# Kernel optimization log

Measured on AMD Instinct MI355X. Metric: run time of the kernel, lower is better.

The kernel has to match this reference:

```python
import jax, jax.numpy as jnp
import numpy as np
import math

D_MODEL = 1024
NUM_HEADS = 16
D_K = D_MODEL // NUM_HEADS
SEQ = 4096
THETA = 10000.0


def _rope_tables(d_k, max_seq_len, theta):
    freqs = 1.0 / theta ** (jnp.arange(0, d_k, 2, dtype=jnp.float32) / d_k)  # (d_k/2,)
    pos = jnp.arange(max_seq_len, dtype=jnp.float32)
    ang = pos[:, None] * freqs[None, :]  # (S, d_k/2)
    return jnp.cos(ang), jnp.sin(ang)


def setup_inputs() -> dict:
    key = jax.random.key(0)
    ks = jax.random.split(key, 5)
    std = math.sqrt(2.0 / (D_MODEL + D_MODEL))
    def trunc_w(k):
        return jax.random.truncated_normal(k, -3.0, 3.0, (D_MODEL, D_MODEL), jnp.float32) * std
    x = jax.random.normal(ks[0], (1, SEQ, D_MODEL), jnp.float32)
    Wq, Wk, Wv, Wo = trunc_w(ks[1]), trunc_w(ks[2]), trunc_w(ks[3]), trunc_w(ks[4])
    cos, sin = _rope_tables(D_K, SEQ, THETA)
    positions = jnp.arange(SEQ, dtype=jnp.int32)
    return {"x": x, "Wq": Wq, "Wk": Wk, "Wv": Wv, "Wo": Wo,
            "cos": cos, "sin": sin, "positions": positions}


def _apply_rope(t, cos, sin, positions):
    # t: (b, h, s, d_k); cos/sin: (max_s, d_k/2)
    c = cos[positions][None, None]  # (1,1,s,d_k/2)
    s = sin[positions][None, None]
    x1, x2 = t[..., ::2], t[..., 1::2]
    rotated = jnp.stack([x1 * c - x2 * s, x1 * s + x2 * c], axis=-1)  # (b,h,s,d_k/2,2)
    return rotated.reshape(t.shape)


def reference(x, Wq, Wk, Wv, Wo, cos, sin, positions):
    b, s, d = x.shape
    h, dk = NUM_HEADS, D_K
    def proj(W):
        y = jnp.einsum('bsi,oi->bso', x, W)
        return y.reshape(b, s, h, dk).transpose(0, 2, 1, 3)  # (b,h,s,dk)
    Q, K, V = proj(Wq), proj(Wk), proj(Wv)
    Q = _apply_rope(Q, cos, sin, positions)
    K = _apply_rope(K, cos, sin, positions)
    scores = jnp.einsum('bhqd,bhkd->bhqk', Q, K) / math.sqrt(dk)
    causal = jnp.tril(jnp.ones((s, s), dtype=bool))
    scores = jnp.where(causal[None, None], scores, -jnp.inf)
    weights = jax.nn.softmax(scores, axis=-1)
    y = jnp.einsum('bhqk,bhkd->bhqd', weights, V)
    y = y.transpose(0, 2, 1, 3).reshape(b, s, d)
    return jnp.einsum('bsi,oi->bso', y, Wo)
```

## Files before the change

### kernel.cpp

```cpp
#include <hip/hip_runtime.h>
#include <math.h>

#define SEQ 4096
#define DM  1024
#define NH  16
#define DK  64

typedef __attribute__((ext_vector_type(4))) float f32x4;
typedef __attribute__((ext_vector_type(8))) short bf16x8;
typedef __attribute__((ext_vector_type(8))) unsigned short u16x8;

union FragU { u16x8 u; bf16x8 b; ushort4 q[2]; unsigned w[4]; };

__device__ __forceinline__ unsigned cvtpk(float a, float b) {
    unsigned r; asm("v_cvt_pk_bf16_f32 %0, %1, %2" : "=v"(r) : "v"(a), "v"(b)); return r;
}
__device__ __forceinline__ float fexp2(float x) {
    float r; asm("v_exp_f32 %0, %1" : "=v"(r) : "v"(x)); return r;
}
__device__ __forceinline__ void split4(float4 v, ushort4& hv, ushort4& lv) {
    union { ushort4 q; unsigned w[2]; } H, L;
    H.w[0] = cvtpk(v.x, v.y); H.w[1] = cvtpk(v.z, v.w);
    const float rx = v.x - __uint_as_float(H.w[0] << 16);
    const float ry = v.y - __uint_as_float(H.w[0] & 0xffff0000u);
    const float rz = v.z - __uint_as_float(H.w[1] << 16);
    const float rw = v.w - __uint_as_float(H.w[1] & 0xffff0000u);
    L.w[0] = cvtpk(rx, ry); L.w[1] = cvtpk(rz, rw);
    hv = H.q; lv = L.q;
}
__device__ __forceinline__ void split1(float f, unsigned short& h, unsigned short& l) {
    const unsigned hw = cvtpk(f, f) & 0xffffu;
    h = (unsigned short)hw;
    const float r = f - __uint_as_float(hw << 16);
    l = (unsigned short)(__float_as_uint(r) >> 16);
}

template<int MODE>
__global__ __launch_bounds__(256, 2)
void gemm_mfma(const float* __restrict__ Af,
               const unsigned short* __restrict__ Ahi, const unsigned short* __restrict__ Alo,
               const float* __restrict__ W0, const float* __restrict__ W1,
               const float* __restrict__ W2,
               unsigned short* __restrict__ OQh, unsigned short* __restrict__ OQl,
               unsigned short* __restrict__ OKh, unsigned short* __restrict__ OKl,
               unsigned short* __restrict__ OVh, unsigned short* __restrict__ OVl,
               float* __restrict__ Ofp,
               const float* __restrict__ cosT, const float* __restrict__ sinT,
               const int* __restrict__ positions)
{
    constexpr int NT = (MODE == 4) ? 24 : 8;
    __shared__ unsigned short As[128][76];
    __shared__ unsigned short Bs[128][76];

    const int t   = threadIdx.x;
    const int bid = blockIdx.x;
    const int qpx = (32 * NT) >> 3;
    const int swz = (bid & 7) * qpx + (bid >> 3);
    const int by  = swz / NT;
    const int bxf = swz % NT;
    const int wt  = (MODE == 4) ? (bxf >> 3) : 0;
    const int bx  = (MODE == 4) ? (bxf & 7) : bxf;
    const int m0  = by * 128;
    const float* W = (MODE == 4) ? (wt == 0 ? W0 : (wt == 1 ? W1 : W2)) : W0;

    const int lane = t & 63, w = t >> 6;
    const int wr = w >> 1, wc = w & 1;
    const int l15 = lane & 15, lg = lane >> 4;

    const int ar = t >> 1, ah = t & 1;
    const float* Ap = (MODE == 4) ? &Af[(size_t)(m0 + ar) * DM + ah * 16] : nullptr;
    const unsigned short* Aph = (MODE == 0) ? &Ahi[(size_t)(m0 + ar) * DM + ah * 16] : nullptr;
    const unsigned short* Apl = (MODE == 0) ? &Alo[(size_t)(m0 + ar) * DM + ah * 16] : nullptr;
    const float* Wp = &W[(size_t)(bx * 128 + ar) * DM + ah * 16];

    f32x4 acc[4][4];
#pragma unroll
    for (int mi = 0; mi < 4; ++mi)
#pragma unroll
        for (int ni = 0; ni < 4; ++ni) acc[mi][ni] = (f32x4){0.f, 0.f, 0.f, 0.f};

    float4 pa[4], pb[4];
    u16x8 pah[2], pal[2];
    if constexpr (MODE == 4) {
#pragma unroll
        for (int g = 0; g < 4; ++g) pa[g] = *reinterpret_cast<const float4*>(Ap + g * 4);
    } else {
        pah[0] = *reinterpret_cast<const u16x8*>(Aph);
        pah[1] = *reinterpret_cast<const u16x8*>(Aph + 8);
        pal[0] = *reinterpret_cast<const u16x8*>(Apl);
        pal[1] = *reinterpret_cast<const u16x8*>(Apl + 8);
    }
#pragma unroll
    for (int g = 0; g < 4; ++g) pb[g] = *reinterpret_cast<const float4*>(Wp + g * 4);

    for (int kt = 0; kt < 32; ++kt) {
        if constexpr (MODE == 4) {
#pragma unroll
            for (int g = 0; g < 4; ++g) {
                ushort4 hv, lv;
                split4(pa[g], hv, lv);
                *reinterpret_cast<ushort4*>(&As[ar][8 * g + 4 * ah])      = hv;
                *reinterpret_cast<ushort4*>(&As[ar][32 + 8 * g + 4 * ah]) = lv;
            }
        } else {
            FragU h0, h1, l0, l1;
            h0.u = pah[0]; h1.u = pah[1]; l0.u = pal[0]; l1.u = pal[1];
            *reinterpret_cast<ushort4*>(&As[ar][0  + 4 * ah]) = h0.q[0];
            *reinterpret_cast<ushort4*>(&As[ar][8  + 4 * ah]) = h0.q[1];
            *reinterpret_cast<ushort4*>(&As[ar][16 + 4 * ah]) = h1.q[0];
            *reinterpret_cast<ushort4*>(&As[ar][24 + 4 * ah]) = h1.q[1];
            *reinterpret_cast<ushort4*>(&As[ar][32 + 4 * ah]) = l0.q[0];
            *reinterpret_cast<ushort4*>(&As[ar][40 + 4 * ah]) = l0.q[1];
            *reinterpret_cast<ushort4*>(&As[ar][48 + 4 * ah]) = l1.q[0];
            *reinterpret_cast<ushort4*>(&As[ar][56 + 4 * ah]) = l1.q[1];
        }
#pragma unroll
        for (int g = 0; g < 4; ++g) {
            ushort4 hv, lv;
            split4(pb[g], hv, lv);
            *reinterpret_cast<ushort4*>(&Bs[ar][8 * g + 4 * ah])      = hv;
            *reinterpret_cast<ushort4*>(&Bs[ar][32 + 8 * g + 4 * ah]) = lv;
        }
        __syncthreads();

        if (kt < 31) {
            const int ko = (kt + 1) * 32;
            if constexpr (MODE == 4) {
#pragma unroll
                for (int g = 0; g < 4; ++g)
                    pa[g] = *reinterpret_cast<const float4*>(Ap + ko + g * 4);
            } else {
                pah[0] = *reinterpret_cast<const u16x8*>(Aph + ko);
                pah[1] = *reinterpret_cast<const u16x8*>(Aph + ko + 8);
                pal[0] = *reinterpret_cast<const u16x8*>(Apl + ko);
                pal[1] = *reinterpret_cast<const u16x8*>(Apl + ko + 8);
            }
#pragma unroll
            for (int g = 0; g < 4; ++g)
                pb[g] = *reinterpret_cast<const float4*>(Wp + ko + g * 4);
        }

        FragU b_h[4], b_l[4];
#pragma unroll
        for (int ni = 0; ni < 4; ++ni) {
            const int row = wc * 64 + ni * 16 + l15;
            b_h[ni].u = *reinterpret_cast<const u16x8*>(&Bs[row][8 * lg]);
            b_l[ni].u = *reinterpret_cast<const u16x8*>(&Bs[row][32 + 8 * lg]);
        }
#pragma unroll
        for (int mi = 0; mi < 4; ++mi) {
            FragU a_h, a_l;
            const int row = wr * 64 + mi * 16 + l15;
            a_h.u = *reinterpret_cast<const u16x8*>(&As[row][8 * lg]);
            a_l.u = *reinterpret_cast<const u16x8*>(&As[row][32 + 8 * lg]);
#pragma unroll
            for (int ni = 0; ni < 4; ++ni) {
                f32x4 c = acc[mi][ni];
                c = __builtin_amdgcn_mfma_f32_16x16x32_bf16(a_h.b, b_h[ni].b, c, 0, 0, 0);
                c = __builtin_amdgcn_mfma_f32_16x16x32_bf16(a_h.b, b_l[ni].b, c, 0, 0, 0);
                c = __builtin_amdgcn_mfma_f32_16x16x32_bf16(a_l.b, b_h[ni].b, c, 0, 0, 0);
                acc[mi][ni] = c;
            }
        }
        __syncthreads();
    }

    if constexpr (MODE == 0) {
#pragma unroll
        for (int mi = 0; mi < 4; ++mi)
#pragma unroll
            for (int ni = 0; ni < 4; ++ni)
#pragma unroll
                for (int r = 0; r < 4; ++r) {
                    const int m = m0 + wr * 64 + mi * 16 + lg * 4 + r;
                    const int n = bx * 128 + wc * 64 + ni * 16 + l15;
                    Ofp[(size_t)m * DM + n] = acc[mi][ni][r];
                }
    } else if (wt == 2) {
#pragma unroll
        for (int mi = 0; mi < 4; ++mi)
#pragma unroll
            for (int ni = 0; ni < 4; ++ni) {
                ushort4 hv, lv;
                unsigned short* hp = (unsigned short*)&hv;
                unsigned short* lp = (unsigned short*)&lv;
#pragma unroll
                for (int r = 0; r < 4; ++r) split1(acc[mi][ni][r], hp[r], lp[r]);
                const int vrow = bx * 128 + wc * 64 + ni * 16 + l15;
                const size_t off = (size_t)vrow * SEQ + m0 + wr * 64 + mi * 16 + lg * 4;
                *reinterpret_cast<ushort4*>(&OVh[off]) = hv;
                *reinterpret_cast<ushort4*>(&OVl[off]) = lv;
            }
    } else {
        unsigned short* Oh = (wt == 0) ? OQh : OKh;
        unsigned short* Ol = (wt == 0) ? OQl : OKl;
        const int head = bx * 2 + wc;
        const float qsc = 0.1803368801f;
#pragma unroll
        for (int mi = 0; mi < 4; ++mi)
#pragma unroll
            for (int r = 0; r < 4; ++r) {
                const int m   = m0 + wr * 64 + mi * 16 + lg * 4 + r;
                const int pos = positions[m];
#pragma unroll
                for (int ni = 0; ni < 4; ++ni) {
                    float val = acc[mi][ni][r];
                    const int d = ni * 16 + l15;
                    const float other = __shfl_xor(val, 1);
                    const float cc = cosT[pos * 32 + ni * 8 + (l15 >> 1)];
                    const float ss = sinT[pos * 32 + ni * 8 + (l15 >> 1)];
                    val = (d & 1) ? fmaf(other, ss, val * cc)
                                  : fmaf(other, -ss, val * cc);
                    if (wt == 0) val *= qsc;
                    unsigned short hh, ll;
                    split1(val, hh, ll);
                    const size_t off = ((size_t)head * SEQ + m) * DK + d;
                    Oh[off] = hh; Ol[off] = ll;
                }
            }
    }
}

__global__ __launch_bounds__(256, 1)
void attn_mfma(const unsigned short* __restrict__ Qhi, const unsigned short* __restrict__ Qlo,
               const unsigned short* __restrict__ Khi, const unsigned short* __restrict__ Klo,
               const unsigned short* __restrict__ Vhi, const unsigned short* __restrict__ Vlo,
               unsigned short* __restrict__ Yh, unsigned short* __restrict__ Yl)
{
    __shared__ unsigned short KsH[64][72], KsL[64][72];
    __shared__ unsigned short VsH[64][72], VsL[64][72];

    const int t = threadIdx.x, lane = t & 63, w = t >> 6;
    const int bid = blockIdx.x;
    const int xcd = bid & 7, idx = bid >> 3;
    const int h = 2 * xcd + (idx >> 4);
    const int pairI = idx & 15;
    const int l15 = lane & 15, lg = lane >> 4, dg = lg * 4;
    const int srow = t >> 2, q16 = t & 3;
    const int sc0 = (q16 >> 1) * 32 + 4 * (q16 & 1);

    u16x8 pf[8];

#pragma unroll 1
    for (int pass = 0; pass < 2; ++pass) {
        const int qt = pass ? (31 - pairI) : pairI;
        const int K0 = 2 * qt;
        const int ktmax = K0 + 1;

        bf16x8 qh[2][2], ql[2][2];
#pragma unroll
        for (int u = 0; u < 2; ++u) {
            const size_t qrow = ((size_t)h * SEQ + (size_t)qt * 128 + u * 64 + w * 16 + l15) * DK;
#pragma unroll
            for (int c = 0; c < 2; ++c) {
                FragU uh, ul;
                uh.q[0] = *reinterpret_cast<const ushort4*>(&Qhi[qrow + c * 32 + dg]);
                uh.q[1] = *reinterpret_cast<const ushort4*>(&Qhi[qrow + c * 32 + 16 + dg]);
                ul.q[0] = *reinterpret_cast<const ushort4*>(&Qlo[qrow + c * 32 + dg]);
                ul.q[1] = *reinterpret_cast<const ushort4*>(&Qlo[qrow + c * 32 + 16 + dg]);
                qh[u][c] = uh.b; ql[u][c] = ul.b;
            }
        }

        f32x4 yacc[2][4];
#pragma unroll
        for (int u = 0; u < 2; ++u)
#pragma unroll
            for (int dt = 0; dt < 4; ++dt) yacc[u][dt] = (f32x4){0.f, 0.f, 0.f, 0.f};
        float m_run[2] = {-1e30f, -1e30f}, l_run[2] = {0.f, 0.f};

        {
            const size_t gK = ((size_t)h * SEQ + srow) * DK + q16 * 16;
            const size_t gV = ((size_t)h * DK + srow) * SEQ + q16 * 16;
            pf[0] = *reinterpret_cast<const u16x8*>(&Khi[gK]);
            pf[1] = *reinterpret_cast<const u16x8*>(&Khi[gK + 8]);
            pf[2] = *reinterpret_cast<const u16x8*>(&Klo[gK]);
            pf[3] = *reinterpret_cast<const u16x8*>(&Klo[gK + 8]);
            pf[4] = *reinterpret_cast<const u16x8*>(&Vhi[gV]);
            pf[5] = *reinterpret_cast<const u16x8*>(&Vhi[gV + 8]);
            pf[6] = *reinterpret_cast<const u16x8*>(&Vlo[gV]);
            pf[7] = *reinterpret_cast<const u16x8*>(&Vlo[gV + 8]);
        }

        for (int kt = 0; kt <= ktmax; ++kt) {
            __syncthreads();
            {
                FragU f0, f1;
                f0.u = pf[0]; f1.u = pf[1];
                *reinterpret_cast<ushort4*>(&KsH[srow][sc0])      = f0.q[0];
                *reinterpret_cast<ushort4*>(&KsH[srow][sc0 + 8])  = f0.q[1];
                *reinterpret_cast<ushort4*>(&KsH[srow][sc0 + 16]) = f1.q[0];
                *reinterpret_cast<ushort4*>(&KsH[srow][sc0 + 24]) = f1.q[1];
                f0.u = pf[2]; f1.u = pf[3];
                *reinterpret_cast<ushort4*>(&KsL[srow][sc0])      = f0.q[0];
                *reinterpret_cast<ushort4*>(&KsL[srow][sc0 + 8])  = f0.q[1];
                *reinterpret_cast<ushort4*>(&KsL[srow][sc0 + 16]) = f1.q[0];
                *reinterpret_cast<ushort4*>(&KsL[srow][sc0 + 24]) = f1.q[1];
                f0.u = pf[4]; f1.u = pf[5];
                *reinterpret_cast<ushort4*>(&VsH[srow][sc0])      = f0.q[0];
                *reinterpret_cast<ushort4*>(&VsH[srow][sc0 + 8])  = f0.q[1];
                *reinterpret_cast<ushort4*>(&VsH[srow][sc0 + 16]) = f1.q[0];
                *reinterpret_cast<ushort4*>(&VsH[srow][sc0 + 24]) = f1.q[1];
                f0.u = pf[6]; f1.u = pf[7];
                *reinterpret_cast<ushort4*>(&VsL[srow][sc0])      = f0.q[0];
                *reinterpret_cast<ushort4*>(&VsL[srow][sc0 + 8])  = f0.q[1];
                *reinterpret_cast<ushort4*>(&VsL[srow][sc0 + 16]) = f1.q[0];
                *reinterpret_cast<ushort4*>(&VsL[srow][sc0 + 24]) = f1.q[1];
            }
            __syncthreads();

            if (kt < ktmax) {
                const size_t gK = ((size_t)h * SEQ + (size_t)(kt + 1) * 64 + srow) * DK + q16 * 16;
                const size_t gV = ((size_t)h * DK + srow) * SEQ + (size_t)(kt + 1) * 64 + q16 * 16;
                pf[0] = *reinterpret_cast<const u16x8*>(&Khi[gK]);
                pf[1] = *reinterpret_cast<const u16x8*>(&Khi[gK + 8]);
                pf[2] = *reinterpret_cast<const u16x8*>(&Klo[gK]);
                pf[3] = *reinterpret_cast<const u16x8*>(&Klo[gK + 8]);
                pf[4] = *reinterpret_cast<const u16x8*>(&Vhi[gV]);
                pf[5] = *reinterpret_cast<const u16x8*>(&Vhi[gV + 8]);
                pf[6] = *reinterpret_cast<const u16x8*>(&Vlo[gV]);
                pf[7] = *reinterpret_cast<const u16x8*>(&Vlo[gV + 8]);
            }

            const int mode0 = (kt < K0) ? 1 : ((kt == K0) ? 2 : 0);
            const int mode1 = (kt <= K0) ? 1 : 2;
            const bool act0 = (mode0 != 0);

            f32x4 st0[4], st1[4];
#pragma unroll
            for (int ktile = 0; ktile < 4; ++ktile) {
                const bool sk0 = !act0 || (mode0 == 2 && ktile > w);
                const bool sk1 = (mode1 == 2 && ktile > w);
                f32x4 s0 = (f32x4){0.f, 0.f, 0.f, 0.f};
                f32x4 s1 = (f32x4){0.f, 0.f, 0.f, 0.f};
                if (!sk0 || !sk1) {
#pragma unroll
                    for (int c = 0; c < 2; ++c) {
                        FragU kh, kl;
                        kh.u = *reinterpret_cast<const u16x8*>(&KsH[ktile * 16 + l15][c * 32 + 8 * lg]);
                        kl.u = *reinterpret_cast<const u16x8*>(&KsL[ktile * 16 + l15][c * 32 + 8 * lg]);
                        if (!sk0) {
                            s0 = __builtin_amdgcn_mfma_f32_16x16x32_bf16(kh.b, qh[0][c], s0, 0, 0, 0);
                            s0 = __builtin_amdgcn_mfma_f32_16x16x32_bf16(kh.b, ql[0][c], s0, 0, 0, 0);
                            s0 = __builtin_amdgcn_mfma_f32_16x16x32_bf16(kl.b, qh[0][c], s0, 0, 0, 0);
                        }
                        if (!sk1) {
                            s1 = __builtin_amdgcn_mfma_f32_16x16x32_bf16(kh.b, qh[1][c], s1, 0, 0, 0);
                            s1 = __builtin_amdgcn_mfma_f32_16x16x32_bf16(kh.b, ql[1][c], s1, 0, 0, 0);
                            s1 = __builtin_amdgcn_mfma_f32_16x16x32_bf16(kl.b, qh[1][c], s1, 0, 0, 0);
                        }
                    }
                }
                st0[ktile] = sk0 ? (f32x4){-1e30f, -1e30f, -1e30f, -1e30f} : s0;
                st1[ktile] = sk1 ? (f32x4){-1e30f, -1e30f, -1e30f, -1e30f} : s1;
            }

            if (mode0 == 2) {
#pragma unroll
                for (int ktile = 0; ktile < 4; ++ktile)
#pragma unroll
                    for (int r = 0; r < 4; ++r)
                        if (ktile * 16 + dg + r > w * 16 + l15) st0[ktile][r] = -1e30f;
            }
            if (mode1 == 2) {
#pragma unroll
                for (int ktile = 0; ktile < 4; ++ktile)
#pragma unroll
                    for (int r = 0; r < 4; ++r)
                        if (ktile * 16 + dg + r > w * 16 + l15) st1[ktile][r] = -1e30f;
            }

            bf16x8 pa0[2], pa1[2];
#pragma unroll
            for (int u = 0; u < 2; ++u) {
                if (u == 0 && !act0) continue;
                f32x4* st = (u == 0) ? st0 : st1;
                float rowmax = st[0][0];
#pragma unroll
                for (int ktile = 0; ktile < 4; ++ktile)
#pragma unroll
                    for (int r = 0; r < 4; ++r) rowmax = fmaxf(rowmax, st[ktile][r]);
                rowmax = fmaxf(rowmax, __shfl_xor(rowmax, 16));
                rowmax = fmaxf(rowmax, __shfl_xor(rowmax, 32));
                if (!__all(rowmax <= m_run[u] + 11.5f)) {
                    const float mnew = fmaxf(m_run[u], rowmax);
                    const float factor = fexp2(m_run[u] - mnew);
                    l_run[u] *= factor;
#pragma unroll
                    for (int r = 0; r < 4; ++r) {
                        const float fr = __shfl(factor, (lg << 2) | r);
#pragma unroll
                        for (int dt = 0; dt < 4; ++dt) yacc[u][dt][r] *= fr;
                    }
                    m_run[u] = mnew;
                }
                float p[4][4]; float psum = 0.f;
#pragma unroll
                for (int ktile = 0; ktile < 4; ++ktile)
#pragma unroll
                    for (int r = 0; r < 4; ++r) {
                        p[ktile][r] = fexp2(st[ktile][r] - m_run[u]);
                        psum += p[ktile][r];
                    }
                psum += __shfl_xor(psum, 16);
                psum += __shfl_xor(psum, 32);
                l_run[u] += psum;
#pragma unroll
                for (int c = 0; c < 2; ++c) {
                    FragU P;
                    P.w[0] = cvtpk(p[2 * c][0],     p[2 * c][1]);
                    P.w[1] = cvtpk(p[2 * c][2],     p[2 * c][3]);
                    P.w[2] = cvtpk(p[2 * c + 1][0], p[2 * c + 1][1]);
                    P.w[3] = cvtpk(p[2 * c + 1][2], p[2 * c + 1][3]);
                    if (u == 0) pa0[c] = P.b; else pa1[c] = P.b;
                }
            }

#pragma unroll
            for (int dt = 0; dt < 4; ++dt) {
#pragma unroll
                for (int c = 0; c < 2; ++c) {
                    FragU vh, vl;
                    vh.u = *reinterpret_cast<const u16x8*>(&VsH[dt * 16 + l15][c * 32 + 8 * lg]);
                    vl.u = *reinterpret_cast<const u16x8*>(&VsL[dt * 16 + l15][c * 32 + 8 * lg]);
                    if (act0) {
                        yacc[0][dt] = __builtin_amdgcn_mfma_f32_16x16x32_bf16(pa0[c], vh.b, yacc[0][dt], 0, 0, 0);
                        yacc[0][dt] = __builtin_amdgcn_mfma_f32_16x16x32_bf16(pa0[c], vl.b, yacc[0][dt], 0, 0, 0);
                    }
                    yacc[1][dt] = __builtin_amdgcn_mfma_f32_16x16x32_bf16(pa1[c], vh.b, yacc[1][dt], 0, 0, 0);
                    yacc[1][dt] = __builtin_amdgcn_mfma_f32_16x16x32_bf16(pa1[c], vl.b, yacc[1][dt], 0, 0, 0);
                }
            }
        }

#pragma unroll
        for (int u = 0; u < 2; ++u) {
            const float inv = 1.0f / l_run[u];
#pragma unroll
            for (int r = 0; r < 4; ++r) {
                const float ir = __shfl(inv, (lg << 2) | r);
                const size_t row = (size_t)qt * 128 + u * 64 + w * 16 + lg * 4 + r;
#pragma unroll
                for (int dt = 0; dt < 4; ++dt) {
                    unsigned short hh, ll;
                    split1(yacc[u][dt][r] * ir, hh, ll);
                    const size_t off = row * DM + h * DK + dt * 16 + l15;
                    Yh[off] = hh; Yl[off] = ll;
                }
            }
        }
    }
}

extern "C" void kernel_launch(void* const* d_in, const int* in_sizes, int n_in,
                              void* d_out, int out_size, void* d_ws, size_t ws_size,
                              hipStream_t stream)
{
    const float* x    = (const float*)d_in[0];
    const float* Wq   = (const float*)d_in[1];
    const float* Wk   = (const float*)d_in[2];
    const float* Wv   = (const float*)d_in[3];
    const float* Wo   = (const float*)d_in[4];
    const float* cosT = (const float*)d_in[5];
    const float* sinT = (const float*)d_in[6];
    const int*   pos  = (const int*)d_in[7];
    float* out = (float*)d_out;

    const size_t E = (size_t)SEQ * DM;
    unsigned short* qh = (unsigned short*)d_ws;
    unsigned short* ql = qh + E;
    unsigned short* kh = ql + E;
    unsigned short* kl = kh + E;
    unsigned short* vh = kl + E;
    unsigned short* vl = vh + E;
    unsigned short* yh = vl + E;
    unsigned short* yl = yh + E;

    gemm_mfma<4><<<dim3(768), dim3(256), 0, stream>>>(
        x, nullptr, nullptr, Wq, Wk, Wv,
        qh, ql, kh, kl, vh, vl, nullptr, cosT, sinT, pos);
    attn_mfma<<<dim3(256), dim3(256), 0, stream>>>(qh, ql, kh, kl, vh, vl, yh, yl);
    gemm_mfma<0><<<dim3(256), dim3(256), 0, stream>>>(
        nullptr, yh, yl, Wo, nullptr, nullptr,
        nullptr, nullptr, nullptr, nullptr, nullptr, nullptr, out, cosT, sinT, pos);
}
```

Baseline: 258.9 us.

## Split attention into one q-tile per block with XOR-swizzled LDS and occupancy 2

The attention kernel drops the two-pass paired q-tile loop. It launches 512 blocks, one per (head, q-tile), ordered from the longest causal tile first, and raises launch bounds to two blocks per CU. Unpadded LDS tiles use an XOR swizzle on the column groups to avoid bank conflicts, and s_setprio raises wave priority around the MFMA sections. This trades the explicit load balance of pairing short and long tiles for more concurrent blocks, and relies on the longest-first ordering to balance the tail. The 2-block bound may also limit registers.

```diff
diff --git a/kernel.cpp b/kernel.cpp
--- a/kernel.cpp
+++ b/kernel.cpp
@@ -221,57 +221,103 @@
     }
 }
 
-__global__ __launch_bounds__(256, 1)
+__global__ __launch_bounds__(256, 2)
 void attn_mfma(const unsigned short* __restrict__ Qhi, const unsigned short* __restrict__ Qlo,
                const unsigned short* __restrict__ Khi, const unsigned short* __restrict__ Klo,
                const unsigned short* __restrict__ Vhi, const unsigned short* __restrict__ Vlo,
                unsigned short* __restrict__ Yh, unsigned short* __restrict__ Yl)
 {
-    __shared__ unsigned short KsH[64][72], KsL[64][72];
-    __shared__ unsigned short VsH[64][72], VsL[64][72];
+    __shared__ unsigned short KsH[64][64], KsL[64][64];
+    __shared__ unsigned short VsH[64][64], VsL[64][64];
 
     const int t = threadIdx.x, lane = t & 63, w = t >> 6;
     const int bid = blockIdx.x;
-    const int xcd = bid & 7, idx = bid >> 3;
-    const int h = 2 * xcd + (idx >> 4);
-    const int pairI = idx & 15;
+    const int xcd = bid & 7, r_ = bid >> 3;
+    const int h  = 2 * xcd + (r_ & 1);
+    const int qt = 31 - (r_ >> 1);
     const int l15 = lane & 15, lg = lane >> 4, dg = lg * 4;
     const int srow = t >> 2, q16 = t & 3;
-    const int sc0 = (q16 >> 1) * 32 + 4 * (q16 & 1);
+
+    int wcol[4];
+#pragma unroll
+    for (int m = 0; m < 4; ++m) {
+        const int g = (q16 >> 1) * 4 + m;
+        wcol[m] = (((g ^ (srow & 7)) << 3) + ((q16 & 1) << 2));
+    }
+
+    const int K0 = 2 * qt;
+    const int ktmax = K0 + 1;
+
+    bf16x8 qh[2][2], ql[2][2];
+#pragma unroll
+    for (int u = 0; u < 2; ++u) {
+        const size_t qrow = ((size_t)h * SEQ + (size_t)qt * 128 + u * 64 + w * 16 + l15) * DK;
+#pragma unroll
+        for (int c = 0; c < 2; ++c) {
+            FragU uh, ul;
+            uh.q[0] = *reinterpret_cast<const ushort4*>(&Qhi[qrow + c * 32 + dg]);
+            uh.q[1] = *reinterpret_cast<const ushort4*>(&Qhi[qrow + c * 32 + 16 + dg]);
+            ul.q[0] = *reinterpret_cast<const ushort4*>(&Qlo[qrow + c * 32 + dg]);
+            ul.q[1] = *reinterpret_cast<const ushort4*>(&Qlo[qrow + c * 32 + 16 + dg]);
+            qh[u][c] = uh.b; ql[u][c] = ul.b;
+        }
+    }
+
+    f32x4 yacc[2][4];
+#pragma unroll
+    for (int u = 0; u < 2; ++u)
+#pragma unroll
+        for (int dt = 0; dt < 4; ++dt) yacc[u][dt] = (f32x4){0.f, 0.f, 0.f, 0.f};
+    float m_run[2] = {-1e30f, -1e30f}, l_run[2] = {0.f, 0.f};
 
     u16x8 pf[8];
-
-#pragma unroll 1
-    for (int pass = 0; pass < 2; ++pass) {
-        const int qt = pass ? (31 - pairI) : pairI;
-        const int K0 = 2 * qt;
-        const int ktmax = K0 + 1;
-
-        bf16x8 qh[2][2], ql[2][2];
-#pragma unroll
-        for (int u = 0; u < 2; ++u) {
-            const size_t qrow = ((size_t)h * SEQ + (size_t)qt * 128 + u * 64 + w * 16 + l15) * DK;
-#pragma unroll
-            for (int c = 0; c < 2; ++c) {
-                FragU uh, ul;
-                uh.q[0] = *reinterpret_cast<const ushort4*>(&Qhi[qrow + c * 32 + dg]);
-                uh.q[1] = *reinterpret_cast<const ushort4*>(&Qhi[qrow + c * 32 + 16 + dg]);
-                ul.q[0] = *reinterpret_cast<const ushort4*>(&Qlo[qrow + c * 32 + dg]);
-                ul.q[1] = *reinterpret_cast<const ushort4*>(&Qlo[qrow + c * 32 + 16 + dg]);
-                qh[u][c] = uh.b; ql[u][c] = ul.b;
-            }
-        }
-
-        f32x4 yacc[2][4];
-#pragma unroll
-        for (int u = 0; u < 2; ++u)
-#pragma unroll
-            for (int dt = 0; dt < 4; ++dt) yacc[u][dt] = (f32x4){0.f, 0.f, 0.f, 0.f};
-        float m_run[2] = {-1e30f, -1e30f}, l_run[2] = {0.f, 0.f};
-
+    {
+        const size_t gK = ((size_t)h * SEQ + srow) * DK + q16 * 16;
+        const size_t gV = ((size_t)h * DK + srow) * SEQ + q16 * 16;
+        pf[0] = *reinterpret_cast<const u16x8*>(&Khi[gK]);
+        pf[1] = *reinterpret_cast<const u16x8*>(&Khi[gK + 8]);
+        pf[2] = *reinterpret_cast<const u16x8*>(&Klo[gK]);
+        pf[3] = *reinterpret_cast<const u16x8*>(&Klo[gK + 8]);
+        pf[4] = *reinterpret_cast<const u16x8*>(&Vhi[gV]);
+        pf[5] = *reinterpret_cast<const u16x8*>(&Vhi[gV + 8]);
+        pf[6] = *reinterpret_cast<const u16x8*>(&Vlo[gV]);
+        pf[7] = *reinterpret_cast<const u16x8*>(&Vlo[gV + 8]);
+    }
+
+    for (int kt = 0; kt <= ktmax; ++kt) {
+        __syncthreads();
         {
-            const size_t gK = ((size_t)h * SEQ + srow) * DK + q16 * 16;
-            const size_t gV = ((size_t)h * DK + srow) * SEQ + q16 * 16;
+            FragU f;
+            f.u = pf[0];
+            *reinterpret_cast<ushort4*>(&KsH[srow][wcol[0]]) = f.q[0];
+            *reinterpret_cast<ushort4*>(&KsH[srow][wcol[1]]) = f.q[1];
+            f.u = pf[1];
+            *reinterpret_cast<ushort4*>(&KsH[srow][wcol[2]]) = f.q[0];
+            *reinterpret_cast<ushort4*>(&KsH[srow][wcol[3]]) = f.q[1];
+            f.u = pf[2];
+            *reinterpret_cast<ushort4*>(&KsL[srow][wcol[0]]) = f.q[0];
+            *reinterpret_cast<ushort4*>(&KsL[srow][wcol[1]]) = f.q[1];
+            f.u = pf[3];
+            *reinterpret_cast<ushort4*>(&KsL[srow][wcol[2]]) = f.q[0];
+            *reinterpret_cast<ushort4*>(&KsL[srow][wcol[3]]) = f.q[1];
+            f.u = pf[4];
+            *reinterpret_cast<ushort4*>(&VsH[srow][wcol[0]]) = f.q[0];
+            *reinterpret_cast<ushort4*>(&VsH[srow][wcol[1]]) = f.q[1];
+            f.u = pf[5];
+            *reinterpret_cast<ushort4*>(&VsH[srow][wcol[2]]) = f.q[0];
+            *reinterpret_cast<ushort4*>(&VsH[srow][wcol[3]]) = f.q[1];
+            f.u = pf[6];
+            *reinterpret_cast<ushort4*>(&VsL[srow][wcol[0]]) = f.q[0];
+            *reinterpret_cast<ushort4*>(&VsL[srow][wcol[1]]) = f.q[1];
+            f.u = pf[7];
+            *reinterpret_cast<ushort4*>(&VsL[srow][wcol[2]]) = f.q[0];
+            *reinterpret_cast<ushort4*>(&VsL[srow][wcol[3]]) = f.q[1];
+        }
+        __syncthreads();
+
+        if (kt < ktmax) {
+            const size_t gK = ((size_t)h * SEQ + (size_t)(kt + 1) * 64 + srow) * DK + q16 * 16;
+            const size_t gV = ((size_t)h * DK + srow) * SEQ + (size_t)(kt + 1) * 64 + q16 * 16;
             pf[0] = *reinterpret_cast<const u16x8*>(&Khi[gK]);
             pf[1] = *reinterpret_cast<const u16x8*>(&Khi[gK + 8]);
             pf[2] = *reinterpret_cast<const u16x8*>(&Klo[gK]);
@@ -282,171 +328,140 @@
             pf[7] = *reinterpret_cast<const u16x8*>(&Vlo[gV + 8]);
         }
 
-        for (int kt = 0; kt <= ktmax; ++kt) {
-            __syncthreads();
-            {
-                FragU f0, f1;
-                f0.u = pf[0]; f1.u = pf[1];
-                *reinterpret_cast<ushort4*>(&KsH[srow][sc0])      = f0.q[0];
-                *reinterpret_cast<ushort4*>(&KsH[srow][sc0 + 8])  = f0.q[1];
-                *reinterpret_cast<ushort4*>(&KsH[srow][sc0 + 16]) = f1.q[0];
-                *reinterpret_cast<ushort4*>(&KsH[srow][sc0 + 24]) = f1.q[1];
-                f0.u = pf[2]; f1.u = pf[3];
-                *reinterpret_cast<ushort4*>(&KsL[srow][sc0])      = f0.q[0];
-                *reinterpret_cast<ushort4*>(&KsL[srow][sc0 + 8])  = f0.q[1];
-                *reinterpret_cast<ushort4*>(&KsL[srow][sc0 + 16]) = f1.q[0];
-                *reinterpret_cast<ushort4*>(&KsL[srow][sc0 + 24]) = f1.q[1];
-                f0.u = pf[4]; f1.u = pf[5];
-                *reinterpret_cast<ushort4*>(&VsH[srow][sc0])      = f0.q[0];
-                *reinterpret_cast<ushort4*>(&VsH[srow][sc0 + 8])  = f0.q[1];
-                *reinterpret_cast<ushort4*>(&VsH[srow][sc0 + 16]) = f1.q[0];
-                *reinterpret_cast<ushort4*>(&VsH[srow][sc0 + 24]) = f1.q[1];
-                f0.u = pf[6]; f1.u = pf[7];
-                *reinterpret_cast<ushort4*>(&VsL[srow][sc0])      = f0.q[0];
-                *reinterpret_cast<ushort4*>(&VsL[srow][sc0 + 8])  = f0.q[1];
-                *reinterpret_cast<ushort4*>(&VsL[srow][sc0 + 16]) = f1.q[0];
-                *reinterpret_cast<ushort4*>(&VsL[srow][sc0 + 24]) = f1.q[1];
-            }
-            __syncthreads();
-
-            if (kt < ktmax) {
-                const size_t gK = ((size_t)h * SEQ + (size_t)(kt + 1) * 64 + srow) * DK + q16 * 16;
-                const size_t gV = ((size_t)h * DK + srow) * SEQ + (size_t)(kt + 1) * 64 + q16 * 16;
-                pf[0] = *reinterpret_cast<const u16x8*>(&Khi[gK]);
-                pf[1] = *reinterpret_cast<const u16x8*>(&Khi[gK + 8]);
-                pf[2] = *reinterpret_cast<const u16x8*>(&Klo[gK]);
-                pf[3] = *reinterpret_cast<const u16x8*>(&Klo[gK + 8]);
-                pf[4] = *reinterpret_cast<const u16x8*>(&Vhi[gV]);
-                pf[5] = *reinterpret_cast<const u16x8*>(&Vhi[gV + 8]);
-                pf[6] = *reinterpret_cast<const u16x8*>(&Vlo[gV]);
-                pf[7] = *reinterpret_cast<const u16x8*>(&Vlo[gV + 8]);
-            }
-
-            const int mode0 = (kt < K0) ? 1 : ((kt == K0) ? 2 : 0);
-            const int mode1 = (kt <= K0) ? 1 : 2;
-            const bool act0 = (mode0 != 0);
-
-            f32x4 st0[4], st1[4];
-#pragma unroll
-            for (int ktile = 0; ktile < 4; ++ktile) {
-                const bool sk0 = !act0 || (mode0 == 2 && ktile > w);
-                const bool sk1 = (mode1 == 2 && ktile > w);
-                f32x4 s0 = (f32x4){0.f, 0.f, 0.f, 0.f};
-                f32x4 s1 = (f32x4){0.f, 0.f, 0.f, 0.f};
-                if (!sk0 || !sk1) {
-#pragma unroll
-                    for (int c = 0; c < 2; ++c) {
-                        FragU kh, kl;
-                        kh.u = *reinterpret_cast<const u16x8*>(&KsH[ktile * 16 + l15][c * 32 + 8 * lg]);
-                        kl.u = *reinterpret_cast<const u16x8*>(&KsL[ktile * 16 + l15][c * 32 + 8 * lg]);
-                        if (!sk0) {
-                            s0 = __builtin_amdgcn_mfma_f32_16x16x32_bf16(kh.b, qh[0][c], s0, 0, 0, 0);
-                            s0 = __builtin_amdgcn_mfma_f32_16x16x32_bf16(kh.b, ql[0][c], s0, 0, 0, 0);
-                            s0 = __builtin_amdgcn_mfma_f32_16x16x32_bf16(kl.b, qh[0][c], s0, 0, 0, 0);
-                        }
-                        if (!sk1) {
-                            s1 = __builtin_amdgcn_mfma_f32_16x16x32_bf16(kh.b, qh[1][c], s1, 0, 0, 0);
-                            s1 = __builtin_amdgcn_mfma_f32_16x16x32_bf16(kh.b, ql[1][c], s1, 0, 0, 0);
-                            s1 = __builtin_amdgcn_mfma_f32_16x16x32_bf16(kl.b, qh[1][c], s1, 0, 0, 0);
-                        }
+        const int mode0 = (kt < K0) ? 1 : ((kt == K0) ? 2 : 0);
+        const int mode1 = (kt <= K0) ? 1 : 2;
+        const bool act0 = (mode0 != 0);
+
+        f32x4 st0[4], st1[4];
+        __builtin_amdgcn_s_setprio(1);
+#pragma unroll
+        for (int ktile = 0; ktile < 4; ++ktile) {
+            const bool sk0 = !act0 || (mode0 == 2 && ktile > w);
+            const bool sk1 = (mode1 == 2 && ktile > w);
+            f32x4 s0 = (f32x4){0.f, 0.f, 0.f, 0.f};
+            f32x4 s1 = (f32x4){0.f, 0.f, 0.f, 0.f};
+            if (!sk0 || !sk1) {
+                const int rowK = ktile * 16 + l15;
+                const int swk  = rowK & 7;
+#pragma unroll
+                for (int c = 0; c < 2; ++c) {
+                    FragU kh, kl;
+                    const int pcol = ((c * 4 + lg) ^ swk) << 3;
+                    kh.u = *reinterpret_cast<const u16x8*>(&KsH[rowK][pcol]);
+                    kl.u = *reinterpret_cast<const u16x8*>(&KsL[rowK][pcol]);
+                    if (!sk0) {
+                        s0 = __builtin_amdgcn_mfma_f32_16x16x32_bf16(kh.b, qh[0][c], s0, 0, 0, 0);
+                        s0 = __builtin_amdgcn_mfma_f32_16x16x32_bf16(kh.b, ql[0][c], s0, 0, 0, 0);
+                        s0 = __builtin_amdgcn_mfma_f32_16x16x32_bf16(kl.b, qh[0][c], s0, 0, 0, 0);
+                    }
+                    if (!sk1) {
+                        s1 = __builtin_amdgcn_mfma_f32_16x16x32_bf16(kh.b, qh[1][c], s1, 0, 0, 0);
+                        s1 = __builtin_amdgcn_mfma_f32_16x16x32_bf16(kh.b, ql[1][c], s1, 0, 0, 0);
+                        s1 = __builtin_amdgcn_mfma_f32_16x16x32_bf16(kl.b, qh[1][c], s1, 0, 0, 0);
                     }
                 }
-                st0[ktile] = sk0 ? (f32x4){-1e30f, -1e30f, -1e30f, -1e30f} : s0;
-                st1[ktile] = sk1 ? (f32x4){-1e30f, -1e30f, -1e30f, -1e30f} : s1;
-            }
-
-            if (mode0 == 2) {
-#pragma unroll
-                for (int ktile = 0; ktile < 4; ++ktile)
-#pragma unroll
-                    for (int r = 0; r < 4; ++r)
-                        if (ktile * 16 + dg + r > w * 16 + l15) st0[ktile][r] = -1e30f;
-            }
-            if (mode1 == 2) {
-#pragma unroll
-                for (int ktile = 0; ktile < 4; ++ktile)
-#pragma unroll
-                    for (int r = 0; r < 4; ++r)
-                        if (ktile * 16 + dg + r > w * 16 + l15) st1[ktile][r] = -1e30f;
-            }
-
-            bf16x8 pa0[2], pa1[2];
-#pragma unroll
-            for (int u = 0; u < 2; ++u) {
-                if (u == 0 && !act0) continue;
-                f32x4* st = (u == 0) ? st0 : st1;
-                float rowmax = st[0][0];
-#pragma unroll
-                for (int ktile = 0; ktile < 4; ++ktile)
-#pragma unroll
-                    for (int r = 0; r < 4; ++r) rowmax = fmaxf(rowmax, st[ktile][r]);
-                rowmax = fmaxf(rowmax, __shfl_xor(rowmax, 16));
-                rowmax = fmaxf(rowmax, __shfl_xor(rowmax, 32));
-                if (!__all(rowmax <= m_run[u] + 11.5f)) {
-                    const float mnew = fmaxf(m_run[u], rowmax);
-                    const float factor = fexp2(m_run[u] - mnew);
-                    l_run[u] *= factor;
-#pragma unroll
-                    for (int r = 0; r < 4; ++r) {
-                        const float fr = __shfl(factor, (lg << 2) | r);
-#pragma unroll
-                        for (int dt = 0; dt < 4; ++dt) yacc[u][dt][r] *= fr;
-                    }
-                    m_run[u] = mnew;
+            }
+            st0[ktile] = sk0 ? (f32x4){-1e30f, -1e30f, -1e30f, -1e30f} : s0;
+            st1[ktile] = sk1 ? (f32x4){-1e30f, -1e30f, -1e30f, -1e30f} : s1;
+        }
+        __builtin_amdgcn_s_setprio(0);
+
+        if (mode0 == 2) {
+#pragma unroll
+            for (int ktile = 0; ktile < 4; ++ktile)
+#pragma unroll
+                for (int r = 0; r < 4; ++r)
+                    if (ktile * 16 + dg + r > w * 16 + l15) st0[ktile][r] = -1e30f;
+        }
+        if (mode1 == 2) {
+#pragma unroll
+            for (int ktile = 0; ktile < 4; ++ktile)
+#pragma unroll
+                for (int r = 0; r < 4; ++r)
+                    if (ktile * 16 + dg + r > w * 16 + l15) st1[ktile][r] = -1e30f;
+        }
+
+        bf16x8 pa0[2], pa1[2];
+#pragma unroll
+        for (int u = 0; u < 2; ++u) {
+            if (u == 0 && !act0) continue;
+            f32x4* st = (u == 0) ? st0 : st1;
+            float rowmax = st[0][0];
+#pragma unroll
+            for (int ktile = 0; ktile < 4; ++ktile)
+#pragma unroll
+                for (int r = 0; r < 4; ++r) rowmax = fmaxf(rowmax, st[ktile][r]);
+            rowmax = fmaxf(rowmax, __shfl_xor(rowmax, 16));
+            rowmax = fmaxf(rowmax, __shfl_xor(rowmax, 32));
+            if (!__all(rowmax <= m_run[u] + 11.5f)) {
+                const float mnew = fmaxf(m_run[u], rowmax);
+                const float factor = fexp2(m_run[u] - mnew);
+                l_run[u] *= factor;
+#pragma unroll
+                for (int r = 0; r < 4; ++r) {
+                    const float fr = __shfl(factor, (lg << 2) | r);
+#pragma unroll
+                    for (int dt = 0; dt < 4; ++dt) yacc[u][dt][r] *= fr;
                 }
-                float p[4][4]; float psum = 0.f;
-#pragma unroll
-                for (int ktile = 0; ktile < 4; ++ktile)
-#pragma unroll
-                    for (int r = 0; r < 4; ++r) {
-                        p[ktile][r] = fexp2(st[ktile][r] - m_run[u]);
-                        psum += p[ktile][r];
-                    }
-                psum += __shfl_xor(psum, 16);
-                psum += __shfl_xor(psum, 32);
-                l_run[u] += psum;
-#pragma unroll
-                for (int c = 0; c < 2; ++c) {
-                    FragU P;
-                    P.w[0] = cvtpk(p[2 * c][0],     p[2 * c][1]);
-                    P.w[1] = cvtpk(p[2 * c][2],     p[2 * c][3]);
-                    P.w[2] = cvtpk(p[2 * c + 1][0], p[2 * c + 1][1]);
-                    P.w[3] = cvtpk(p[2 * c + 1][2], p[2 * c + 1][3]);
-                    if (u == 0) pa0[c] = P.b; else pa1[c] = P.b;
+                m_run[u] = mnew;
+            }
+            float p[4][4]; float psum = 0.f;
+#pragma unroll
+            for (int ktile = 0; ktile < 4; ++ktile)
+#pragma unroll
+                for (int r = 0; r < 4; ++r) {
+                    p[ktile][r] = fexp2(st[ktile][r] - m_run[u]);
+                    psum += p[ktile][r];
                 }
-            }
-
+            psum += __shfl_xor(psum, 16);
+            psum += __shfl_xor(psum, 32);
+            l_run[u] += psum;
+#pragma unroll
+            for (int c = 0; c < 2; ++c) {
+                FragU P;
+                P.w[0] = cvtpk(p[2 * c][0],     p[2 * c][1]);
+                P.w[1] = cvtpk(p[2 * c][2],     p[2 * c][3]);
+                P.w[2] = cvtpk(p[2 * c + 1][0], p[2 * c + 1][1]);
+                P.w[3] = cvtpk(p[2 * c + 1][2], p[2 * c + 1][3]);
+                if (u == 0) pa0[c] = P.b; else pa1[c] = P.b;
+            }
+        }
+
+        __builtin_amdgcn_s_setprio(1);
+#pragma unroll
+        for (int dt = 0; dt < 4; ++dt) {
+            const int rowV = dt * 16 + l15;
+            const int swv  = rowV & 7;
+#pragma unroll
+            for (int c = 0; c < 2; ++c) {
+                FragU vh, vl;
+                const int pcol = ((c * 4 + lg) ^ swv) << 3;
+                vh.u = *reinterpret_cast<const u16x8*>(&VsH[rowV][pcol]);
+                vl.u = *reinterpret_cast<const u16x8*>(&VsL[rowV][pcol]);
+                if (act0) {
+                    yacc[0][dt] = __builtin_amdgcn_mfma_f32_16x16x32_bf16(pa0[c], vh.b, yacc[0][dt], 0, 0, 0);
+                    yacc[0][dt] = __builtin_amdgcn_mfma_f32_16x16x32_bf16(pa0[c], vl.b, yacc[0][dt], 0, 0, 0);
+                }
+                yacc[1][dt] = __builtin_amdgcn_mfma_f32_16x16x32_bf16(pa1[c], vh.b, yacc[1][dt], 0, 0, 0);
+                yacc[1][dt] = __builtin_amdgcn_mfma_f32_16x16x32_bf16(pa1[c], vl.b, yacc[1][dt], 0, 0, 0);
+            }
+        }
+        __builtin_amdgcn_s_setprio(0);
+    }
+
+#pragma unroll
+    for (int u = 0; u < 2; ++u) {
+        const float inv = 1.0f / l_run[u];
+#pragma unroll
+        for (int r = 0; r < 4; ++r) {
+            const float ir = __shfl(inv, (lg << 2) | r);
+            const size_t row = (size_t)qt * 128 + u * 64 + w * 16 + lg * 4 + r;
 #pragma unroll
             for (int dt = 0; dt < 4; ++dt) {
-#pragma unroll
-                for (int c = 0; c < 2; ++c) {
-                    FragU vh, vl;
-                    vh.u = *reinterpret_cast<const u16x8*>(&VsH[dt * 16 + l15][c * 32 + 8 * lg]);
-                    vl.u = *reinterpret_cast<const u16x8*>(&VsL[dt * 16 + l15][c * 32 + 8 * lg]);
-                    if (act0) {
-                        yacc[0][dt] = __builtin_amdgcn_mfma_f32_16x16x32_bf16(pa0[c], vh.b, yacc[0][dt], 0, 0, 0);
-                        yacc[0][dt] = __builtin_amdgcn_mfma_f32_16x16x32_bf16(pa0[c], vl.b, yacc[0][dt], 0, 0, 0);
-                    }
-                    yacc[1][dt] = __builtin_amdgcn_mfma_f32_16x16x32_bf16(pa1[c], vh.b, yacc[1][dt], 0, 0, 0);
-                    yacc[1][dt] = __builtin_amdgcn_mfma_f32_16x16x32_bf16(pa1[c], vl.b, yacc[1][dt], 0, 0, 0);
-                }
-            }
-        }
-
-#pragma unroll
-        for (int u = 0; u < 2; ++u) {
-            const float inv = 1.0f / l_run[u];
-#pragma unroll
-            for (int r = 0; r < 4; ++r) {
-                const float ir = __shfl(inv, (lg << 2) | r);
-                const size_t row = (size_t)qt * 128 + u * 64 + w * 16 + lg * 4 + r;
-#pragma unroll
-                for (int dt = 0; dt < 4; ++dt) {
-                    unsigned short hh, ll;
-                    split1(yacc[u][dt][r] * ir, hh, ll);
-                    const size_t off = row * DM + h * DK + dt * 16 + l15;
-                    Yh[off] = hh; Yl[off] = ll;
-                }
+                unsigned short hh, ll;
+                split1(yacc[u][dt][r] * ir, hh, ll);
+                const size_t off = row * DM + h * DK + dt * 16 + l15;
+                Yh[off] = hh; Yl[off] = ll;
             }
         }
     }
@@ -479,7 +494,7 @@
     gemm_mfma<4><<<dim3(768), dim3(256), 0, stream>>>(
         x, nullptr, nullptr, Wq, Wk, Wv,
         qh, ql, kh, kl, vh, vl, nullptr, cosT, sinT, pos);
-    attn_mfma<<<dim3(256), dim3(256), 0, stream>>>(qh, ql, kh, kl, vh, vl, yh, yl);
+    attn_mfma<<<dim3(512), dim3(256), 0, stream>>>(qh, ql, kh, kl, vh, vl, yh, yl);
     gemm_mfma<0><<<dim3(256), dim3(256), 0, stream>>>(
         nullptr, yh, yl, Wo, nullptr, nullptr,
         nullptr, nullptr, nullptr, nullptr, nullptr, nullptr, out, cosT, sinT, pos);
```

New measurement: 284.6 us. 9.9% more time.
